# Performance work log

Hardware: AMD Instinct MI355X
Metric: run time of the kernel (lower is better)

## Reference

```python
import jax, jax.numpy as jnp
import numpy as np

B, T = 8, 5
C2, C1, C0 = 128, 256, 512  # in_channels = [C2, C1, C0]


def _ln(x, g, b):
    # LayerNorm over last (channel) axis
    m = jnp.mean(x, axis=-1, keepdims=True)
    v = jnp.var(x, axis=-1, keepdims=True)
    return (x - m) * jax.lax.rsqrt(v + 1e-5) * g + b


def _fuse_branch(x, gc, bc, gr, br, Wcur, Wref, bf, convw, bns, bnb):
    # x: [B, C, T, H, W]
    xt = jnp.transpose(x, (0, 2, 3, 4, 1))            # [B, T, H, W, C] (channel-last, like the permutes)
    cur = xt[:, -1]                                    # [B, H, W, C] last frame
    refs = xt[:, :-1]                                  # [B, T-1, H, W, C]
    # ShiftVSS stand-in: cross-frame fuse with residual (vectorized over T-1 frames)
    cur_proj = jnp.einsum('bhwc,cd->bhwd', _ln(cur, gc, bc), Wcur)        # [B,H,W,C]
    ref_proj = jnp.einsum('bthwc,cd->bthwd', _ln(refs, gr, br), Wref)     # [B,T-1,H,W,C]
    h = cur[:, None] + jax.nn.silu(cur_proj[:, None] + ref_proj + bf)     # [B,T-1,H,W,C]
    # BaseConv 1x1: pointwise conv + folded-BN + SiLU
    y = jax.nn.silu(jnp.einsum('bthwc,cd->bthwd', h, convw) * bns + bnb)  # [B,T-1,H,W,C]
    # fused temporal max + avg pooling (AdaptiveMax/AvgPool3d to T=1)
    pooled = jnp.max(y, axis=1) + jnp.mean(y, axis=1)                     # [B,H,W,C]
    return jnp.transpose(pooled, (0, 3, 1, 2))                            # [B,C,H,W]


def setup_inputs() -> dict:
    key = jax.random.key(0)
    ks = jax.random.split(key, 32)

    def n(k, shape, s=1.0):
        return jax.random.normal(k, shape, dtype=jnp.float32) * s

    d = {}
    d['x2'] = n(ks[0], (B, C2, T, 64, 64))
    d['x1'] = n(ks[1], (B, C1, T, 32, 32))
    d['x0'] = n(ks[2], (B, C0, T, 16, 16))  # unused by forward, kept for signature fidelity
    for i, (p, C) in enumerate([('2', C2), ('1', C1)]):
        o = 3 + i * 4
        d[f'g{p}c'] = jnp.ones((C,), jnp.float32)
        d[f'b{p}c'] = jnp.zeros((C,), jnp.float32)
        d[f'g{p}r'] = jnp.ones((C,), jnp.float32)
        d[f'b{p}r'] = jnp.zeros((C,), jnp.float32)
        d[f'W{p}cur'] = n(ks[o], (C, C), 0.02)
        d[f'W{p}ref'] = n(ks[o + 1], (C, C), 0.02)
        d[f'bias{p}'] = jnp.zeros((C,), jnp.float32)
        d[f'convw{p}'] = n(ks[o + 2], (C, C), 0.02)
        d[f'bns{p}'] = jnp.ones((C,), jnp.float32)
        d[f'bnb{p}'] = jnp.zeros((C,), jnp.float32)
    return d


def reference(x2, x1, x0,
              g2c, b2c, g2r, b2r, W2cur, W2ref, bias2, convw2, bns2, bnb2,
              g1c, b1c, g1r, b1r, W1cur, W1ref, bias1, convw1, bns1, bnb1):
    x2_out = _fuse_branch(x2, g2c, b2c, g2r, b2r, W2cur, W2ref, bias2, convw2, bns2, bnb2)
    x1_out = _fuse_branch(x1, g1c, b1c, g1r, b1r, W1cur, W1ref, bias1, convw1, bns1, bnb1)
    return (x2_out, x1_out)
```

## Files before the change

kernel.cpp:

```cpp
#include <hip/hip_runtime.h>
#include <stdint.h>

#define DI __device__ __forceinline__

typedef __attribute__((ext_vector_type(8))) short short8;
typedef __attribute__((ext_vector_type(4))) float f32x4;

DI float bf2f(unsigned short u){ union{unsigned int i; float f;} v; v.i = ((unsigned int)u)<<16; return v.f; }
DI unsigned short f2bf(float f){ union{float f; unsigned int i;} v; v.f=f; return (unsigned short)((v.i + 0x7fffu + ((v.i>>16)&1u))>>16); }
DI float siluf(float x){ return x/(1.f + __expf(-x)); }
DI f32x4 vzero(){ f32x4 z; z[0]=0.f;z[1]=0.f;z[2]=0.f;z[3]=0.f; return z; }
DI f32x4 vsplat(float x){ f32x4 z; z[0]=x;z[1]=x;z[2]=x;z[3]=x; return z; }

struct PrepArgs {
  const float* W[6];
  const float* g[6];
  unsigned short* Wt[6];
  int C[6];
};

__global__ __launch_bounds__(256) void prep_transpose(PrepArgs a){
  int m = blockIdx.z;
  int C = a.C[m];
  int nt = C >> 5;
  if ((int)blockIdx.x >= nt || (int)blockIdx.y >= nt) return;
  __shared__ float tile[32][33];
  int col = threadIdx.x & 31;
  int rr  = threadIdx.x >> 5;
  const float* W = a.W[m];
  const float* g = a.g[m];
  #pragma unroll
  for (int p=0;p<4;++p){
    int r = rr + p*8;
    int cK = blockIdx.x*32 + r;
    int dN = blockIdx.y*32 + col;
    float v = W[(size_t)cK*C + dN];
    if (g) v *= g[cK];
    tile[r][col] = v;
  }
  __syncthreads();
  unsigned short* Wt = a.Wt[m];
  #pragma unroll
  for (int p=0;p<4;++p){
    int r = rr + p*8;
    int dN = blockIdx.y*32 + r;
    int cK = blockIdx.x*32 + col;
    Wt[(size_t)dN*C + cK] = f2bf(tile[col][r]);
  }
}

struct ColArgs {
  const float* W[4]; const float* g[4]; const float* b[4]; const float* extra[4];
  float* ocs[4]; float* obs[4]; int C[4];
};

__global__ __launch_bounds__(256) void prep_colsum(ColArgs a){
  int j = blockIdx.y;
  int C = a.C[j];
  int d0 = blockIdx.x * 64;
  if (d0 >= C) return;
  int dl = threadIdx.x & 63;
  int g  = threadIdx.x >> 6;
  int d  = d0 + dl;
  const float* W = a.W[j]; const float* gv = a.g[j]; const float* bv = a.b[j];
  float cs = 0.f, bs = 0.f;
  for (int c = g; c < C; c += 4){
    float gc = gv[c], bc = bv[c];
    float w = W[(size_t)c*C + d];
    cs += gc*w;
    bs += bc*w;
  }
  __shared__ float rcs[4][64], rbs[4][64];
  rcs[g][dl] = cs; rbs[g][dl] = bs;
  __syncthreads();
  if (threadIdx.x < 64){
    float c0 = rcs[0][dl]+rcs[1][dl]+rcs[2][dl]+rcs[3][dl];
    float b0 = rbs[0][dl]+rbs[1][dl]+rbs[2][dl]+rbs[3][dl];
    if (a.extra[j]) b0 += a.extra[j][d];
    a.ocs[j][d] = c0;
    a.obs[j][d] = b0;
  }
}

template<int C, int PX>
__global__ __launch_bounds__(512) void fusedv3(
    const float* __restrict__ x,
    const unsigned short* __restrict__ WtCur,
    const unsigned short* __restrict__ WtRef,
    const unsigned short* __restrict__ WtConv,
    const float* __restrict__ colC, const float* __restrict__ biasC,
    const float* __restrict__ colR, const float* __restrict__ biasR,
    const float* __restrict__ bns, const float* __restrict__ bnb,
    float* __restrict__ out, int HW){
  constexpr int T = 5;
  constexpr int WCN = C/32;
  constexpr int MROWS = PX/(8/WCN);
  constexpr int MF = MROWS/16;
  constexpr int KC = C/64;
  constexpr int G = 512/PX;
  constexpr int PER = (C/8)/G;
  constexpr int ABYTES = PX*C*2;
  constexpr int BBYTES = C*128;
  constexpr int LDS_TOT = ABYTES + BBYTES + 4096 + 2*PX*4;
  static_assert(PX*(C+1)*4 <= ABYTES + BBYTES + 4096, "pool fits");

  __shared__ __align__(16) char L[LDS_TOT];
  char* Bsb = L + ABYTES;
  float* red = (float*)(L + ABYTES + BBYTES);
  float* smean = (float*)(L + ABYTES + BBYTES + 4096);
  float* srstd = smean + PX;

  int px0 = blockIdx.x*PX;
  int b = px0 / HW, hw0 = px0 % HW;
  int tid = threadIdx.x, lane = tid&63, wid = tid>>6;
  int wc = wid % WCN, wr = wid / WCN;
  int cl = lane&15, hi = lane>>4;
  const float* xbase = x + (size_t)b*C*T*HW + hw0;

  auto stageXf = [&](const float* xb){
    #pragma unroll
    for (int i=0;i<(C*PX/2048);++i){
      int c, pq;
      if constexpr (C==128){ c = wid*16 + cl; pq = i*4 + hi; }
      else                 { c = wid*32 + i*16 + cl; pq = hi; }
      f32x4 v = *(const f32x4*)(xb + (size_t)c*(T*HW) + pq*4);
      #pragma unroll
      for (int j=0;j<4;++j){
        int px = pq*4 + j;
        *(unsigned short*)(L + px*(2*C) + (((c>>3) ^ (px&7))*16) + (c&7)*2) = f2bf(v[j]);
      }
    }
  };

  auto statsXf = [&](){
    int px = tid & (PX-1), g = tid / PX;
    float s=0.f, q=0.f;
    #pragma unroll
    for (int k2=0;k2<PER;++k2){
      int ch = g*PER + k2;
      short8 v = *(const short8*)(L + px*(2*C) + ((ch ^ (px&7))*16));
      #pragma unroll
      for (int e=0;e<8;++e){ float f = bf2f((unsigned short)v[e]); s += f; q += f*f; }
    }
    red[g*PX+px] = s; red[512 + g*PX+px] = q;
    __syncthreads();
    if (tid < PX){
      float ss=0.f, qq=0.f;
      #pragma unroll
      for (int gg=0; gg<G; ++gg){ ss += red[gg*PX+tid]; qq += red[512+gg*PX+tid]; }
      float m = ss*(1.f/C);
      float var = fmaxf(qq*(1.f/C) - m*m, 0.f);
      smean[tid] = m;
      srstd[tid] = rsqrtf(var + 1e-5f);
    }
    __syncthreads();
  };

  auto stageWf = [&](const unsigned short* Wt, int kc){
    #pragma unroll
    for (int it=0; it<C/64; ++it){
      int i = tid + it*512, row = i>>3, ch = i&7;
      short8 v = *(const short8*)(Wt + (size_t)row*C + kc*64 + ch*8);
      *(short8*)(Bsb + row*128 + ((ch ^ (row&7))*16)) = v;
    }
  };

  auto gemmKCf = [&](f32x4 (&acc)[MF][2], int kc){
    #pragma unroll
    for (int ks=0;ks<2;++ks){
      short8 af[MF], bf8[2];
      #pragma unroll
      for (int mf=0;mf<MF;++mf){
        int row = wr*MROWS + mf*16 + cl;
        int chs = kc*8 + ((ks*4 + hi) ^ (row&7));
        af[mf] = *(const short8*)(L + row*(2*C) + chs*16);
      }
      #pragma unroll
      for (int nf=0;nf<2;++nf){
        int row = wc*32 + nf*16 + cl;
        int chs = (ks*4 + hi) ^ (row&7);
        bf8[nf] = *(const short8*)(Bsb + row*128 + chs*16);
      }
      #pragma unroll
      for (int mf=0;mf<MF;++mf)
        #pragma unroll
        for (int nf=0;nf<2;++nf)
          acc[mf][nf] = __builtin_amdgcn_mfma_f32_16x16x32_bf16(af[mf], bf8[nf], acc[mf][nf], 0,0,0);
    }
  };

  float csR[2], biR[2], scn[2], sbn[2];
  #pragma unroll
  for (int nf=0;nf<2;++nf){
    int d = wc*32 + nf*16 + cl;
    csR[nf] = colR[d]; biR[nf] = biasR[d];
    scn[nf] = bns[d];  sbn[nf] = bnb[d];
  }
  unsigned short pv[2][MF*4], cvr[2][MF*4];
  f32x4 mx[2][MF], sm[2][MF];
  #pragma unroll
  for (int nf=0;nf<2;++nf)
    #pragma unroll
    for (int mf=0;mf<MF;++mf){ mx[nf][mf] = vsplat(-3.0e38f); sm[nf][mf] = vzero(); }

  stageXf(xbase + (size_t)(T-1)*HW);
  __syncthreads();
  statsXf();
  {
    f32x4 acc[MF][2];
    #pragma unroll
    for (int mf=0;mf<MF;++mf){ acc[mf][0]=vzero(); acc[mf][1]=vzero(); }
    #pragma unroll
    for (int kc=0;kc<KC;++kc){
      stageWf(WtCur, kc);
      __syncthreads();
      gemmKCf(acc, kc);
      __syncthreads();
    }
    #pragma unroll
    for (int nf=0;nf<2;++nf){
      int dg = wc*32 + nf*16 + cl;
      float cs = colC[dg], bi = biasC[dg];
      #pragma unroll
      for (int mf=0;mf<MF;++mf)
        #pragma unroll
        for (int r=0;r<4;++r){
          int pl = wr*MROWS + mf*16 + hi*4 + r;
          float P = srstd[pl]*(acc[mf][nf][r] - smean[pl]*cs) + bi;
          pv[nf][mf*4+r] = f2bf(P);
          cvr[nf][mf*4+r] = *(const unsigned short*)(L + pl*(2*C) + (((dg>>3)^(pl&7))*16) + (dg&7)*2);
        }
    }
  }

  for (int t=0;t<4;++t){
    __syncthreads();
    stageXf(xbase + (size_t)t*HW);
    __syncthreads();
    statsXf();

    f32x4 acc[MF][2];
    #pragma unroll
    for (int mf=0;mf<MF;++mf){ acc[mf][0]=vzero(); acc[mf][1]=vzero(); }
    #pragma unroll
    for (int kc=0;kc<KC;++kc){
      stageWf(WtRef, kc);
      __syncthreads();
      gemmKCf(acc, kc);
      __syncthreads();
    }
    #pragma unroll
    for (int nf=0;nf<2;++nf){
      int dg = wc*32 + nf*16 + cl;
      #pragma unroll
      for (int mf=0;mf<MF;++mf)
        #pragma unroll
        for (int r=0;r<4;++r){
          int pl = wr*MROWS + mf*16 + hi*4 + r;
          float pre = srstd[pl]*(acc[mf][nf][r] - smean[pl]*csR[nf]) + biR[nf] + bf2f(pv[nf][mf*4+r]);
          float hv = bf2f(cvr[nf][mf*4+r]) + siluf(pre);
          *(unsigned short*)(L + pl*(2*C) + (((dg>>3)^(pl&7))*16) + (dg&7)*2) = f2bf(hv);
        }
    }
    f32x4 acc2[MF][2];
    #pragma unroll
    for (int mf=0;mf<MF;++mf){ acc2[mf][0]=vzero(); acc2[mf][1]=vzero(); }
    #pragma unroll
    for (int kc=0;kc<KC;++kc){
      stageWf(WtConv, kc);
      __syncthreads();
      gemmKCf(acc2, kc);
      __syncthreads();
    }
    #pragma unroll
    for (int nf=0;nf<2;++nf)
      #pragma unroll
      for (int mf=0;mf<MF;++mf)
        #pragma unroll
        for (int r=0;r<4;++r){
          float y = siluf(acc2[mf][nf][r]*scn[nf] + sbn[nf]);
          mx[nf][mf][r] = fmaxf(mx[nf][mf][r], y);
          sm[nf][mf][r] += y;
        }
  }

  __syncthreads();
  float* pool = (float*)L;
  #pragma unroll
  for (int nf=0;nf<2;++nf){
    int dl = wc*32 + nf*16 + cl;
    #pragma unroll
    for (int mf=0;mf<MF;++mf)
      #pragma unroll
      for (int r=0;r<4;++r){
        int pl = wr*MROWS + mf*16 + hi*4 + r;
        pool[pl*(C+1) + dl] = mx[nf][mf][r] + 0.25f*sm[nf][mf][r];
      }
  }
  __syncthreads();
  constexpr int PQn = PX/4;
  #pragma unroll
  for (int it=0; it<(C*PQn/512); ++it){
    int i = tid + it*512;
    int dl = i / PQn, pq = i % PQn;
    f32x4 vv;
    #pragma unroll
    for (int k=0;k<4;++k) vv[k] = pool[(pq*4+k)*(C+1) + dl];
    *(f32x4*)(out + (size_t)(b*C + dl)*HW + hw0 + pq*4) = vv;
  }
}

extern "C" void kernel_launch(void* const* d_in, const int* in_sizes, int n_in,
                              void* d_out, int out_size, void* d_ws, size_t ws_size,
                              hipStream_t stream) {
  (void)in_sizes; (void)n_in; (void)out_size; (void)ws_size;
  const float* x2    = (const float*)d_in[0];
  const float* x1    = (const float*)d_in[1];
  const float* g2c   = (const float*)d_in[3];
  const float* b2c   = (const float*)d_in[4];
  const float* g2r   = (const float*)d_in[5];
  const float* b2r   = (const float*)d_in[6];
  const float* W2cur = (const float*)d_in[7];
  const float* W2ref = (const float*)d_in[8];
  const float* bias2 = (const float*)d_in[9];
  const float* convw2= (const float*)d_in[10];
  const float* bns2  = (const float*)d_in[11];
  const float* bnb2  = (const float*)d_in[12];
  const float* g1c   = (const float*)d_in[13];
  const float* b1c   = (const float*)d_in[14];
  const float* g1r   = (const float*)d_in[15];
  const float* b1r   = (const float*)d_in[16];
  const float* W1cur = (const float*)d_in[17];
  const float* W1ref = (const float*)d_in[18];
  const float* bias1 = (const float*)d_in[19];
  const float* convw1= (const float*)d_in[20];
  const float* bns1  = (const float*)d_in[21];
  const float* bnb1  = (const float*)d_in[22];

  const int C2 = 128, C1 = 256;
  const int NP2 = 8*64*64, NP1 = 8*32*32;
  const int HW2 = 4096, HW1 = 1024;

  char* ws = (char*)d_ws;
  size_t off = 0;
  auto alloc = [&](size_t bytes){ size_t o = off; off = (off + bytes + 255) & ~(size_t)255; return o; };
  size_t oWtC2 = alloc((size_t)C2*C2*2), oWtR2 = alloc((size_t)C2*C2*2), oWtV2 = alloc((size_t)C2*C2*2);
  size_t oWtC1 = alloc((size_t)C1*C1*2), oWtR1 = alloc((size_t)C1*C1*2), oWtV1 = alloc((size_t)C1*C1*2);
  size_t oColC2 = alloc(C2*4), oBiasC2 = alloc(C2*4), oColR2 = alloc(C2*4), oBiasR2 = alloc(C2*4);
  size_t oColC1 = alloc(C1*4), oBiasC1 = alloc(C1*4), oColR1 = alloc(C1*4), oBiasR1 = alloc(C1*4);

  unsigned short* WtC2 = (unsigned short*)(ws + oWtC2);
  unsigned short* WtR2 = (unsigned short*)(ws + oWtR2);
  unsigned short* WtV2 = (unsigned short*)(ws + oWtV2);
  unsigned short* WtC1 = (unsigned short*)(ws + oWtC1);
  unsigned short* WtR1 = (unsigned short*)(ws + oWtR1);
  unsigned short* WtV1 = (unsigned short*)(ws + oWtV1);
  float* ColC2 = (float*)(ws + oColC2); float* BiasC2 = (float*)(ws + oBiasC2);
  float* ColR2 = (float*)(ws + oColR2); float* BiasR2 = (float*)(ws + oBiasR2);
  float* ColC1 = (float*)(ws + oColC1); float* BiasC1 = (float*)(ws + oBiasC1);
  float* ColR1 = (float*)(ws + oColR1); float* BiasR1 = (float*)(ws + oBiasR1);

  PrepArgs pa;
  pa.W[0]=W2cur;  pa.g[0]=g2c;     pa.Wt[0]=WtC2; pa.C[0]=C2;
  pa.W[1]=W2ref;  pa.g[1]=g2r;     pa.Wt[1]=WtR2; pa.C[1]=C2;
  pa.W[2]=convw2; pa.g[2]=nullptr; pa.Wt[2]=WtV2; pa.C[2]=C2;
  pa.W[3]=W1cur;  pa.g[3]=g1c;     pa.Wt[3]=WtC1; pa.C[3]=C1;
  pa.W[4]=W1ref;  pa.g[4]=g1r;     pa.Wt[4]=WtR1; pa.C[4]=C1;
  pa.W[5]=convw1; pa.g[5]=nullptr; pa.Wt[5]=WtV1; pa.C[5]=C1;
  prep_transpose<<<dim3(8,8,6), 256, 0, stream>>>(pa);

  ColArgs ca;
  ca.W[0]=W2cur; ca.g[0]=g2c; ca.b[0]=b2c; ca.extra[0]=nullptr; ca.ocs[0]=ColC2; ca.obs[0]=BiasC2; ca.C[0]=C2;
  ca.W[1]=W2ref; ca.g[1]=g2r; ca.b[1]=b2r; ca.extra[1]=bias2;   ca.ocs[1]=ColR2; ca.obs[1]=BiasR2; ca.C[1]=C2;
  ca.W[2]=W1cur; ca.g[2]=g1c; ca.b[2]=b1c; ca.extra[2]=nullptr; ca.ocs[2]=ColC1; ca.obs[2]=BiasC1; ca.C[2]=C1;
  ca.W[3]=W1ref; ca.g[3]=g1r; ca.b[3]=b1r; ca.extra[3]=bias1;   ca.ocs[3]=ColR1; ca.obs[3]=BiasR1; ca.C[3]=C1;
  prep_colsum<<<dim3(4, 4), 256, 0, stream>>>(ca);

  float* out2 = (float*)d_out;
  float* out1 = out2 + (size_t)8*C2*HW2;

  fusedv3<128,64><<<NP2/64, 512, 0, stream>>>(
      x2, WtC2, WtR2, WtV2, ColC2, BiasC2, ColR2, BiasR2, bns2, bnb2, out2, HW2);
  fusedv3<256,16><<<NP1/16, 512, 0, stream>>>(
      x1, WtC1, WtR1, WtV1, ColC1, BiasC1, ColR1, BiasR1, bns1, bnb1, out1, HW1);
}
```

Measured before the change: 144.3 us.

## Stage full weight matrices once per GEMM and prefetch next frame into registers

Each weight matrix now goes into LDS whole, replacing the K-chunked staging that needed two barriers per 64-wide chunk, so every GEMM runs with no barriers inside it. The next frame's activations are loaded into registers while the current frame's GEMMs run, hiding global load latency. The warp tiling changes to a 2x4 grid over pixels and output channels, and the C=256 branch now uses 32 pixels per block. In exchange, LDS use per block grows sharply (full CxC bf16 weights), which may lower occupancy, and the prefetch adds register pressure.

Measured after the change: 202.9 us. 1.41x slower.

```diff
diff --git a/kernel.cpp b/kernel.cpp
--- a/kernel.cpp
+++ b/kernel.cpp
@@ -83,7 +83,7 @@
 }
 
 template<int C, int PX>
-__global__ __launch_bounds__(512) void fusedv3(
+__global__ __launch_bounds__(512) void fusedv4(
     const float* __restrict__ x,
     const unsigned short* __restrict__ WtCur,
     const unsigned short* __restrict__ WtRef,
@@ -93,46 +93,55 @@
     const float* __restrict__ bns, const float* __restrict__ bnb,
     float* __restrict__ out, int HW){
   constexpr int T = 5;
-  constexpr int WCN = C/32;
-  constexpr int MROWS = PX/(8/WCN);
+  constexpr int DSPAN = C/4;
+  constexpr int NF = DSPAN/16;
+  constexpr int MROWS = PX/2;
   constexpr int MF = MROWS/16;
-  constexpr int KC = C/64;
+  constexpr int KS = C/32;
   constexpr int G = 512/PX;
   constexpr int PER = (C/8)/G;
-  constexpr int ABYTES = PX*C*2;
-  constexpr int BBYTES = C*128;
-  constexpr int LDS_TOT = ABYTES + BBYTES + 4096 + 2*PX*4;
-  static_assert(PX*(C+1)*4 <= ABYTES + BBYTES + 4096, "pool fits");
+  constexpr int ABYTES = PX*2*C;
+  constexpr int WBYTES = 2*C*C;
+  constexpr int LDS_TOT = ABYTES + WBYTES + 4096 + PX*8;
+  static_assert((size_t)PX*(C+1)*4 <= (size_t)ABYTES + WBYTES, "pool fits");
 
   __shared__ __align__(16) char L[LDS_TOT];
-  char* Bsb = L + ABYTES;
-  float* red = (float*)(L + ABYTES + BBYTES);
-  float* smean = (float*)(L + ABYTES + BBYTES + 4096);
+  char* Ws = L + ABYTES;
+  float* red = (float*)(L + ABYTES + WBYTES);
+  float* smean = (float*)(L + ABYTES + WBYTES + 4096);
   float* srstd = smean + PX;
 
   int px0 = blockIdx.x*PX;
   int b = px0 / HW, hw0 = px0 % HW;
   int tid = threadIdx.x, lane = tid&63, wid = tid>>6;
-  int wc = wid % WCN, wr = wid / WCN;
+  int wr = wid>>2, wc = wid&3;
   int cl = lane&15, hi = lane>>4;
   const float* xbase = x + (size_t)b*C*T*HW + hw0;
 
-  auto stageXf = [&](const float* xb){
-    #pragma unroll
-    for (int i=0;i<(C*PX/2048);++i){
+  auto loadX = [&](const float* xb, f32x4 (&p)[4]){
+    #pragma unroll
+    for (int i=0;i<4;++i){
       int c, pq;
       if constexpr (C==128){ c = wid*16 + cl; pq = i*4 + hi; }
-      else                 { c = wid*32 + i*16 + cl; pq = hi; }
-      f32x4 v = *(const f32x4*)(xb + (size_t)c*(T*HW) + pq*4);
+      else                 { c = wid*32 + (i&1)*16 + cl; pq = (i>>1)*4 + hi; }
+      p[i] = *(const f32x4*)(xb + (size_t)c*(T*HW) + pq*4);
+    }
+  };
+  auto commitX = [&](const f32x4 (&p)[4]){
+    #pragma unroll
+    for (int i=0;i<4;++i){
+      int c, pq;
+      if constexpr (C==128){ c = wid*16 + cl; pq = i*4 + hi; }
+      else                 { c = wid*32 + (i&1)*16 + cl; pq = (i>>1)*4 + hi; }
       #pragma unroll
       for (int j=0;j<4;++j){
         int px = pq*4 + j;
-        *(unsigned short*)(L + px*(2*C) + (((c>>3) ^ (px&7))*16) + (c&7)*2) = f2bf(v[j]);
+        *(unsigned short*)(L + px*(2*C) + (((c>>3) ^ (px&7))*16) + (c&7)*2) = f2bf(p[i][j]);
       }
     }
   };
 
-  auto statsXf = [&](){
+  auto statsX = [&](){
     int px = tid & (PX-1), g = tid / PX;
     float s=0.f, q=0.f;
     #pragma unroll
@@ -156,70 +165,72 @@
     __syncthreads();
   };
 
-  auto stageWf = [&](const unsigned short* Wt, int kc){
-    #pragma unroll
-    for (int it=0; it<C/64; ++it){
-      int i = tid + it*512, row = i>>3, ch = i&7;
-      short8 v = *(const short8*)(Wt + (size_t)row*C + kc*64 + ch*8);
-      *(short8*)(Bsb + row*128 + ((ch ^ (row&7))*16)) = v;
-    }
-  };
-
-  auto gemmKCf = [&](f32x4 (&acc)[MF][2], int kc){
-    #pragma unroll
-    for (int ks=0;ks<2;++ks){
-      short8 af[MF], bf8[2];
+  auto stageW = [&](const unsigned short* Wt){
+    constexpr int CH = C/8;
+    #pragma unroll
+    for (int it=0; it<(C*CH)/512; ++it){
+      int i = tid + it*512, row = i/CH, ch = i%CH;
+      short8 v = *(const short8*)(Wt + (size_t)row*C + ch*8);
+      *(short8*)(Ws + row*(2*C) + ((ch ^ (row&7))*16)) = v;
+    }
+  };
+
+  auto gemm = [&](f32x4 (&acc)[MF][NF]){
+    #pragma unroll
+    for (int ks=0;ks<KS;++ks){
+      short8 af[MF], bf8[NF];
       #pragma unroll
       for (int mf=0;mf<MF;++mf){
         int row = wr*MROWS + mf*16 + cl;
-        int chs = kc*8 + ((ks*4 + hi) ^ (row&7));
+        int chs = (ks*4 + hi) ^ (row&7);
         af[mf] = *(const short8*)(L + row*(2*C) + chs*16);
       }
       #pragma unroll
-      for (int nf=0;nf<2;++nf){
-        int row = wc*32 + nf*16 + cl;
+      for (int nf=0;nf<NF;++nf){
+        int row = wc*DSPAN + nf*16 + cl;
         int chs = (ks*4 + hi) ^ (row&7);
-        bf8[nf] = *(const short8*)(Bsb + row*128 + chs*16);
+        bf8[nf] = *(const short8*)(Ws + row*(2*C) + chs*16);
       }
       #pragma unroll
       for (int mf=0;mf<MF;++mf)
         #pragma unroll
-        for (int nf=0;nf<2;++nf)
+        for (int nf=0;nf<NF;++nf)
           acc[mf][nf] = __builtin_amdgcn_mfma_f32_16x16x32_bf16(af[mf], bf8[nf], acc[mf][nf], 0,0,0);
     }
   };
 
-  float csR[2], biR[2], scn[2], sbn[2];
-  #pragma unroll
-  for (int nf=0;nf<2;++nf){
-    int d = wc*32 + nf*16 + cl;
+  float csR[NF], biR[NF], scn[NF], sbn[NF];
+  #pragma unroll
+  for (int nf=0;nf<NF;++nf){
+    int d = wc*DSPAN + nf*16 + cl;
     csR[nf] = colR[d]; biR[nf] = biasR[d];
     scn[nf] = bns[d];  sbn[nf] = bnb[d];
   }
-  unsigned short pv[2][MF*4], cvr[2][MF*4];
-  f32x4 mx[2][MF], sm[2][MF];
-  #pragma unroll
-  for (int nf=0;nf<2;++nf)
+  unsigned short pv[NF][MF*4], cvr[NF][MF*4];
+  f32x4 mx[NF][MF], sm[NF][MF];
+  #pragma unroll
+  for (int nf=0;nf<NF;++nf)
     #pragma unroll
     for (int mf=0;mf<MF;++mf){ mx[nf][mf] = vsplat(-3.0e38f); sm[nf][mf] = vzero(); }
 
-  stageXf(xbase + (size_t)(T-1)*HW);
-  __syncthreads();
-  statsXf();
+  f32x4 p[4];
+
+  loadX(xbase + (size_t)(T-1)*HW, p);
+  stageW(WtCur);
+  commitX(p);
+  __syncthreads();
+  statsX();
+  loadX(xbase, p);
   {
-    f32x4 acc[MF][2];
-    #pragma unroll
-    for (int mf=0;mf<MF;++mf){ acc[mf][0]=vzero(); acc[mf][1]=vzero(); }
-    #pragma unroll
-    for (int kc=0;kc<KC;++kc){
-      stageWf(WtCur, kc);
-      __syncthreads();
-      gemmKCf(acc, kc);
-      __syncthreads();
-    }
-    #pragma unroll
-    for (int nf=0;nf<2;++nf){
-      int dg = wc*32 + nf*16 + cl;
+    f32x4 acc[MF][NF];
+    #pragma unroll
+    for (int mf=0;mf<MF;++mf)
+      #pragma unroll
+      for (int nf=0;nf<NF;++nf) acc[mf][nf]=vzero();
+    gemm(acc);
+    #pragma unroll
+    for (int nf=0;nf<NF;++nf){
+      int dg = wc*DSPAN + nf*16 + cl;
       float cs = colC[dg], bi = biasC[dg];
       #pragma unroll
       for (int mf=0;mf<MF;++mf)
@@ -235,23 +246,23 @@
 
   for (int t=0;t<4;++t){
     __syncthreads();
-    stageXf(xbase + (size_t)t*HW);
-    __syncthreads();
-    statsXf();
-
-    f32x4 acc[MF][2];
-    #pragma unroll
-    for (int mf=0;mf<MF;++mf){ acc[mf][0]=vzero(); acc[mf][1]=vzero(); }
-    #pragma unroll
-    for (int kc=0;kc<KC;++kc){
-      stageWf(WtRef, kc);
-      __syncthreads();
-      gemmKCf(acc, kc);
-      __syncthreads();
-    }
-    #pragma unroll
-    for (int nf=0;nf<2;++nf){
-      int dg = wc*32 + nf*16 + cl;
+    stageW(WtRef);
+    commitX(p);
+    __syncthreads();
+    statsX();
+    if (t < 3) loadX(xbase + (size_t)(t+1)*HW, p);
+
+    f32x4 acc[MF][NF];
+    #pragma unroll
+    for (int mf=0;mf<MF;++mf)
+      #pragma unroll
+      for (int nf=0;nf<NF;++nf) acc[mf][nf]=vzero();
+    gemm(acc);
+
+    __syncthreads();
+    #pragma unroll
+    for (int nf=0;nf<NF;++nf){
+      int dg = wc*DSPAN + nf*16 + cl;
       #pragma unroll
       for (int mf=0;mf<MF;++mf)
         #pragma unroll
@@ -262,18 +273,17 @@
           *(unsigned short*)(L + pl*(2*C) + (((dg>>3)^(pl&7))*16) + (dg&7)*2) = f2bf(hv);
         }
     }
-    f32x4 acc2[MF][2];
-    #pragma unroll
-    for (int mf=0;mf<MF;++mf){ acc2[mf][0]=vzero(); acc2[mf][1]=vzero(); }
-    #pragma unroll
-    for (int kc=0;kc<KC;++kc){
-      stageWf(WtConv, kc);
-      __syncthreads();
-      gemmKCf(acc2, kc);
-      __syncthreads();
-    }
-    #pragma unroll
-    for (int nf=0;nf<2;++nf)
+    stageW(WtConv);
+    __syncthreads();
+
+    f32x4 acc2[MF][NF];
+    #pragma unroll
+    for (int mf=0;mf<MF;++mf)
+      #pragma unroll
+      for (int nf=0;nf<NF;++nf) acc2[mf][nf]=vzero();
+    gemm(acc2);
+    #pragma unroll
+    for (int nf=0;nf<NF;++nf)
       #pragma unroll
       for (int mf=0;mf<MF;++mf)
         #pragma unroll
@@ -287,8 +297,8 @@
   __syncthreads();
   float* pool = (float*)L;
   #pragma unroll
-  for (int nf=0;nf<2;++nf){
-    int dl = wc*32 + nf*16 + cl;
+  for (int nf=0;nf<NF;++nf){
+    int dl = wc*DSPAN + nf*16 + cl;
     #pragma unroll
     for (int mf=0;mf<MF;++mf)
       #pragma unroll
@@ -300,7 +310,7 @@
   __syncthreads();
   constexpr int PQn = PX/4;
   #pragma unroll
-  for (int it=0; it<(C*PQn/512); ++it){
+  for (int it=0; it<(C*PQn)/512; ++it){
     int i = tid + it*512;
     int dl = i / PQn, pq = i % PQn;
     f32x4 vv;
@@ -379,8 +389,8 @@
   float* out2 = (float*)d_out;
   float* out1 = out2 + (size_t)8*C2*HW2;
 
-  fusedv3<128,64><<<NP2/64, 512, 0, stream>>>(
+  fusedv4<128,64><<<NP2/64, 512, 0, stream>>>(
       x2, WtC2, WtR2, WtV2, ColC2, BiasC2, ColR2, BiasR2, bns2, bnb2, out2, HW2);
-  fusedv3<256,16><<<NP1/16, 512, 0, stream>>>(
+  fusedv4<256,32><<<NP1/32, 512, 0, stream>>>(
       x1, WtC1, WtR1, WtV1, ColC1, BiasC1, ColR1, BiasR1, bns1, bnb1, out1, HW1);
 }
```
